# Optimization experiments

Measured on AMD Instinct MI355X. Metric: run time of the kernel, lower is better.

## Reference

```python
import jax, jax.numpy as jnp
import numpy as np

I, H = 16, 32  # input_size, hidden_size


def _rnn_layer(x, W_ih, W_hh, b_ih, b_hh):
    # x: [B, T, D] -> outputs [B, T, H] of tanh RNN layer
    B, T, _ = x.shape
    # precompute input projection for all timesteps: [B, T, H]
    xp = jnp.einsum('btd,hd->bth', x, W_ih) + b_ih + b_hh

    def step(h, xpt):
        h = jnp.tanh(xpt + h @ W_hh.T)
        return h, h

    h0 = jnp.zeros((B, H), dtype=x.dtype)
    _, ys = jax.lax.scan(step, h0, jnp.swapaxes(xp, 0, 1))  # ys: [T, B, H]
    return jnp.swapaxes(ys, 0, 1)


def setup_inputs() -> dict:
    key = jax.random.key(0)
    ks = jax.random.split(key, 11)
    B, T = 4096, 512
    s0 = 1.0 / np.sqrt(H)  # PyTorch RNN init bound
    u = lambda k, shape: jax.random.uniform(k, shape, jnp.float32, -s0, s0)
    return {
        'x': jax.random.normal(ks[0], (B, T, I), jnp.float32),
        'W_ih0': u(ks[1], (H, I)), 'W_hh0': u(ks[2], (H, H)),
        'b_ih0': u(ks[3], (H,)), 'b_hh0': u(ks[4], (H,)),
        'W_ih1': u(ks[5], (H, H)), 'W_hh1': u(ks[6], (H, H)),
        'b_ih1': u(ks[7], (H,)), 'b_hh1': u(ks[8], (H,)),
        'fc_w': u(ks[9], (1, H)), 'fc_b': u(ks[10], (1,)),
    }


def reference(x, W_ih0, W_hh0, b_ih0, b_hh0, W_ih1, W_hh1, b_ih1, b_hh1, fc_w, fc_b):
    h1 = _rnn_layer(x, W_ih0, W_hh0, b_ih0, b_hh0)   # [B, T, H]
    h2 = _rnn_layer(h1, W_ih1, W_hh1, b_ih1, b_hh1)  # [B, T, H]
    last = h2[:, -1, :]                               # [B, H]
    logits = last @ fc_w.T + fc_b                     # [B, 1]
    return logits
```

## Files before the change

kernel.cpp:

```cpp
#include <hip/hip_runtime.h>

#define T_DIM 512
#define I_DIM 16
#define B_DIM 4096
#define K_CH 32
#define COLS 8
#define SCL 2.885390081777927f

typedef _Float16 f16x8 __attribute__((ext_vector_type(8)));
typedef float f32x4 __attribute__((ext_vector_type(4)));
typedef __fp16 hf2v __attribute__((ext_vector_type(2)));

union Frag { f16x8 v; __fp16 e[8]; uint4 u; };

__device__ __forceinline__ float tanh_s(float u) {
    float e = __builtin_amdgcn_exp2f(u);
    return fmaf(-2.f, __builtin_amdgcn_rcpf(e + 1.f), 1.f);
}

__device__ __forceinline__ f16x8 pack8(float a0, float a1, float a2, float a3,
                                       float b0, float b1, float b2, float b3) {
    Frag f;
    hf2v p0 = __builtin_amdgcn_cvt_pkrtz(a0, a1);
    hf2v p1 = __builtin_amdgcn_cvt_pkrtz(a2, a3);
    hf2v p2 = __builtin_amdgcn_cvt_pkrtz(b0, b1);
    hf2v p3 = __builtin_amdgcn_cvt_pkrtz(b2, b3);
    f.e[0] = p0[0]; f.e[1] = p0[1]; f.e[2] = p1[0]; f.e[3] = p1[1];
    f.e[4] = p2[0]; f.e[5] = p2[1]; f.e[6] = p3[0]; f.e[7] = p3[1];
    return f.v;
}
__device__ __forceinline__ f16x8 tanhpack_s(f32x4 a, f32x4 b) {
    return pack8(tanh_s(a[0]), tanh_s(a[1]), tanh_s(a[2]), tanh_s(a[3]),
                 tanh_s(b[0]), tanh_s(b[1]), tanh_s(b[2]), tanh_s(b[3]));
}
__device__ __forceinline__ f16x8 loadWq32s(const float* W, int row, int g) {
    float4 a = *reinterpret_cast<const float4*>(W + row * 32 + 4 * g);
    float4 b = *reinterpret_cast<const float4*>(W + row * 32 + 16 + 4 * g);
    return pack8(a.x*SCL, a.y*SCL, a.z*SCL, a.w*SCL, b.x*SCL, b.y*SCL, b.z*SCL, b.w*SCL);
}
__device__ __forceinline__ f16x8 loadWq16s(const float* W, int row, int g) {
    float4 a = *reinterpret_cast<const float4*>(W + row * 16 + 4 * g);
    return pack8(a.x*SCL, a.y*SCL, a.z*SCL, a.w*SCL, 0.f, 0.f, 0.f, 0.f);
}

__global__ void __launch_bounds__(128)
rnn2_pc2_kernel(const float* __restrict__ x,
                const float* __restrict__ Wih0, const float* __restrict__ Whh0,
                const float* __restrict__ bih0, const float* __restrict__ bhh0,
                const float* __restrict__ Wih1, const float* __restrict__ Whh1,
                const float* __restrict__ bih1, const float* __restrict__ bhh1,
                const float* __restrict__ fcw, const float* __restrict__ fcb,
                float* __restrict__ out)
{
    const int tid = threadIdx.x;
    const int l   = tid & 63;
    const int wid = tid >> 6;
    const int c   = l & 15;
    const int g   = l >> 4;
    const int rowbase = blockIdx.x * COLS;

    __shared__ __fp16 ring[2][K_CH][64][8];

    f16x8 wT0[2], wT1[2];
    f32x4 bC[2];
    Frag  h1f;
    f32x4 Xacc[2];
    float4 xpA, xpB;
    const float* xlane = nullptr;
    float h20=0.f,h21=0.f,h22=0.f,h23=0.f,h24=0.f,h25=0.f,h26=0.f,h27=0.f;
    Frag h2f; h2f.u = make_uint4(0u, 0u, 0u, 0u);

    if (wid == 0) {
#pragma unroll
        for (int tt = 0; tt < 2; ++tt) {
            const int row = c + 16 * tt;
            wT0[tt] = loadWq32s(Whh0, row, g);
            wT1[tt] = loadWq16s(Wih0, row, g);
            const int r0 = 4 * g + 16 * tt;
            float4 bi = *reinterpret_cast<const float4*>(bih0 + r0);
            float4 bh = *reinterpret_cast<const float4*>(bhh0 + r0);
            bC[tt][0] = (bi.x + bh.x) * SCL; bC[tt][1] = (bi.y + bh.y) * SCL;
            bC[tt][2] = (bi.z + bh.z) * SCL; bC[tt][3] = (bi.w + bh.w) * SCL;
        }
        const size_t xcol = rowbase + (c & (COLS - 1));
        xlane = x + xcol * (size_t)(T_DIM * I_DIM) + 4 * g;
    } else {
#pragma unroll
        for (int tt = 0; tt < 2; ++tt) {
            const int row = c + 16 * tt;
            wT0[tt] = loadWq32s(Wih1, row, g);
            wT1[tt] = loadWq32s(Whh1, row, g);
            const int r0 = 4 * g + 16 * tt;
            float4 bi = *reinterpret_cast<const float4*>(bih1 + r0);
            float4 bh = *reinterpret_cast<const float4*>(bhh1 + r0);
            bC[tt][0] = (bi.x + bh.x) * SCL; bC[tt][1] = (bi.y + bh.y) * SCL;
            bC[tt][2] = (bi.z + bh.z) * SCL; bC[tt][3] = (bi.w + bh.w) * SCL;
        }
    }

#define PSTEP(t, P)                                                                         \
    {                                                                                       \
        f32x4 D0a = __builtin_amdgcn_mfma_f32_16x16x32_f16(wT0[0], h1f.v, Xacc[0], 0,0,0);  \
        f32x4 D0b = __builtin_amdgcn_mfma_f32_16x16x32_f16(wT0[1], h1f.v, Xacc[1], 0,0,0);  \
        Frag xf; xf.v = pack8((P).x, (P).y, (P).z, (P).w, 0.f, 0.f, 0.f, 0.f);              \
        const int tn = ((t) + 3 < T_DIM) ? (t) + 3 : (T_DIM - 1);                           \
        (P) = *reinterpret_cast<const float4*>(xlane + (size_t)tn * I_DIM);                 \
        h1f.v = tanhpack_s(D0a, D0b);                                                       \
        *reinterpret_cast<uint4*>(&ring[((t) / K_CH) & 1][(t) & (K_CH - 1)][l][0]) = h1f.u; \
        Xacc[0] = __builtin_amdgcn_mfma_f32_16x16x32_f16(wT1[0], xf.v, bC[0], 0,0,0);       \
        Xacc[1] = __builtin_amdgcn_mfma_f32_16x16x32_f16(wT1[1], xf.v, bC[1], 0,0,0);       \
    }

#pragma unroll 1
    for (int p = 0; p <= T_DIM / K_CH; ++p) {
        if (wid == 0 && p < T_DIM / K_CH) {
            if (p == 0) {
                float4 x0 = *reinterpret_cast<const float4*>(xlane + 0 * I_DIM);
                Frag xf0; xf0.v = pack8(x0.x, x0.y, x0.z, x0.w, 0.f, 0.f, 0.f, 0.f);
                f32x4 Da = __builtin_amdgcn_mfma_f32_16x16x32_f16(wT1[0], xf0.v, bC[0], 0,0,0);
                f32x4 Db = __builtin_amdgcn_mfma_f32_16x16x32_f16(wT1[1], xf0.v, bC[1], 0,0,0);
                h1f.v = tanhpack_s(Da, Db);
                *reinterpret_cast<uint4*>(&ring[0][0][l][0]) = h1f.u;
                float4 x1 = *reinterpret_cast<const float4*>(xlane + 1 * I_DIM);
                Frag xf1; xf1.v = pack8(x1.x, x1.y, x1.z, x1.w, 0.f, 0.f, 0.f, 0.f);
                Xacc[0] = __builtin_amdgcn_mfma_f32_16x16x32_f16(wT1[0], xf1.v, bC[0], 0,0,0);
                Xacc[1] = __builtin_amdgcn_mfma_f32_16x16x32_f16(wT1[1], xf1.v, bC[1], 0,0,0);
                f32x4 D0a = __builtin_amdgcn_mfma_f32_16x16x32_f16(wT0[0], h1f.v, Xacc[0], 0,0,0);
                f32x4 D0b = __builtin_amdgcn_mfma_f32_16x16x32_f16(wT0[1], h1f.v, Xacc[1], 0,0,0);
                float4 x2 = *reinterpret_cast<const float4*>(xlane + 2 * I_DIM);
                h1f.v = tanhpack_s(D0a, D0b);
                *reinterpret_cast<uint4*>(&ring[0][1][l][0]) = h1f.u;
                Frag xf2; xf2.v = pack8(x2.x, x2.y, x2.z, x2.w, 0.f, 0.f, 0.f, 0.f);
                Xacc[0] = __builtin_amdgcn_mfma_f32_16x16x32_f16(wT1[0], xf2.v, bC[0], 0,0,0);
                Xacc[1] = __builtin_amdgcn_mfma_f32_16x16x32_f16(wT1[1], xf2.v, bC[1], 0,0,0);
                xpA = *reinterpret_cast<const float4*>(xlane + 3 * I_DIM);
                xpB = *reinterpret_cast<const float4*>(xlane + 4 * I_DIM);
#pragma unroll 2
                for (int s = 2; s < K_CH; s += 2) { PSTEP(s, xpA) PSTEP(s + 1, xpB) }
            } else {
                const int t0 = p * K_CH;
#pragma unroll 2
                for (int s = 0; s < K_CH; s += 2) { PSTEP(t0 + s, xpA) PSTEP(t0 + s + 1, xpB) }
            }
        }
        if (wid == 1 && p >= 1) {
            const int cp  = p - 1;
            const int buf = cp & 1;
            Frag hB; hB.u = *reinterpret_cast<const uint4*>(&ring[buf][0][l][0]);
            f32x4 pd1a = __builtin_amdgcn_mfma_f32_16x16x32_f16(wT0[0], hB.v, bC[0], 0,0,0);
            f32x4 pd1b = __builtin_amdgcn_mfma_f32_16x16x32_f16(wT0[1], hB.v, bC[1], 0,0,0);
#pragma unroll 2
            for (int s = 0; s < K_CH; ++s) {
                f32x4 D1a = __builtin_amdgcn_mfma_f32_16x16x32_f16(wT1[0], h2f.v, pd1a, 0,0,0);
                f32x4 D1b = __builtin_amdgcn_mfma_f32_16x16x32_f16(wT1[1], h2f.v, pd1b, 0,0,0);
                const int sn = (s + 1 < K_CH) ? s + 1 : s;
                hB.u = *reinterpret_cast<const uint4*>(&ring[buf][sn][l][0]);
                pd1a = __builtin_amdgcn_mfma_f32_16x16x32_f16(wT0[0], hB.v, bC[0], 0,0,0);
                pd1b = __builtin_amdgcn_mfma_f32_16x16x32_f16(wT0[1], hB.v, bC[1], 0,0,0);
                h20 = tanh_s(D1a[0]); h21 = tanh_s(D1a[1]);
                h22 = tanh_s(D1a[2]); h23 = tanh_s(D1a[3]);
                h24 = tanh_s(D1b[0]); h25 = tanh_s(D1b[1]);
                h26 = tanh_s(D1b[2]); h27 = tanh_s(D1b[3]);
                h2f.v = pack8(h20, h21, h22, h23, h24, h25, h26, h27);
            }
        }
        __syncthreads();
    }
#undef PSTEP

    if (wid == 1) {
        float4 fw0 = *reinterpret_cast<const float4*>(fcw + 4 * g);
        float4 fw1 = *reinterpret_cast<const float4*>(fcw + 16 + 4 * g);
        float part = fw0.x * h20 + fw0.y * h21 + fw0.z * h22 + fw0.w * h23
                   + fw1.x * h24 + fw1.y * h25 + fw1.z * h26 + fw1.w * h27;
        part += __shfl_xor(part, 16, 64);
        part += __shfl_xor(part, 32, 64);
        if (l < COLS) out[rowbase + l] = part + fcb[0];
    }
}

extern "C" void kernel_launch(void* const* d_in, const int* in_sizes, int n_in,
                              void* d_out, int out_size, void* d_ws, size_t ws_size,
                              hipStream_t stream) {
    const float* x    = (const float*)d_in[0];
    const float* Wih0 = (const float*)d_in[1];
    const float* Whh0 = (const float*)d_in[2];
    const float* bih0 = (const float*)d_in[3];
    const float* bhh0 = (const float*)d_in[4];
    const float* Wih1 = (const float*)d_in[5];
    const float* Whh1 = (const float*)d_in[6];
    const float* bih1 = (const float*)d_in[7];
    const float* bhh1 = (const float*)d_in[8];
    const float* fcw  = (const float*)d_in[9];
    const float* fcb  = (const float*)d_in[10];
    float* out = (float*)d_out;

    dim3 grid(B_DIM / COLS);
    rnn2_pc2_kernel<<<grid, 128, 0, stream>>>(x, Wih0, Whh0, bih0, bhh0,
                                              Wih1, Whh1, bih1, bhh1,
                                              fcw, fcb, out);
}
```

Before: 98.02 us.

## Interleave two independent batch groups per wave to hide recurrent latency

Each block now handles 16 batch rows as two independent 8-row chains (A and B), and each wave interleaves the two recurrences so the MFMA and tanh latency of one chain overlaps with the other. The chunk size is halved to 16 so the doubled shared-memory ring stays the same size, and input prefetch depth is raised to four steps per chain. The grid is halved, which reduces the number of waves available to the scheduler and raises register pressure.

```diff
diff --git a/kernel.cpp b/kernel.cpp
--- a/kernel.cpp
+++ b/kernel.cpp
@@ -3,8 +3,9 @@
 #define T_DIM 512
 #define I_DIM 16
 #define B_DIM 4096
-#define K_CH 32
-#define COLS 8
+#define K_CH 16
+#define NCH  (T_DIM / K_CH)
+#define PF   4
 #define SCL 2.885390081777927f
 
 typedef _Float16 f16x8 __attribute__((ext_vector_type(8)));
@@ -17,7 +18,6 @@
     float e = __builtin_amdgcn_exp2f(u);
     return fmaf(-2.f, __builtin_amdgcn_rcpf(e + 1.f), 1.f);
 }
-
 __device__ __forceinline__ f16x8 pack8(float a0, float a1, float a2, float a3,
                                        float b0, float b1, float b2, float b3) {
     Frag f;
@@ -44,31 +44,33 @@
 }
 
 __global__ void __launch_bounds__(128)
-rnn2_pc2_kernel(const float* __restrict__ x,
-                const float* __restrict__ Wih0, const float* __restrict__ Whh0,
-                const float* __restrict__ bih0, const float* __restrict__ bhh0,
-                const float* __restrict__ Wih1, const float* __restrict__ Whh1,
-                const float* __restrict__ bih1, const float* __restrict__ bhh1,
-                const float* __restrict__ fcw, const float* __restrict__ fcb,
-                float* __restrict__ out)
+rnn2_dual_pc_kernel(const float* __restrict__ x,
+                    const float* __restrict__ Wih0, const float* __restrict__ Whh0,
+                    const float* __restrict__ bih0, const float* __restrict__ bhh0,
+                    const float* __restrict__ Wih1, const float* __restrict__ Whh1,
+                    const float* __restrict__ bih1, const float* __restrict__ bhh1,
+                    const float* __restrict__ fcw, const float* __restrict__ fcb,
+                    float* __restrict__ out)
 {
     const int tid = threadIdx.x;
     const int l   = tid & 63;
     const int wid = tid >> 6;
     const int c   = l & 15;
     const int g   = l >> 4;
-    const int rowbase = blockIdx.x * COLS;
-
-    __shared__ __fp16 ring[2][K_CH][64][8];
+    const int rowA = blockIdx.x * 16;
+    __shared__ __fp16 ring[2][2][K_CH][64][8];
 
     f16x8 wT0[2], wT1[2];
     f32x4 bC[2];
-    Frag  h1f;
-    f32x4 Xacc[2];
-    float4 xpA, xpB;
-    const float* xlane = nullptr;
-    float h20=0.f,h21=0.f,h22=0.f,h23=0.f,h24=0.f,h25=0.f,h26=0.f,h27=0.f;
-    Frag h2f; h2f.u = make_uint4(0u, 0u, 0u, 0u);
+    Frag h1A, h1B;
+    f32x4 XaccA[2], XaccB[2];
+    float4 xa0, xa1, xa2, xa3, xb0, xb1, xb2, xb3;
+    const float *xlA = nullptr, *xlB = nullptr;
+    float hA0=0.f,hA1=0.f,hA2=0.f,hA3=0.f,hA4=0.f,hA5=0.f,hA6=0.f,hA7=0.f;
+    float hB0=0.f,hB1=0.f,hB2=0.f,hB3=0.f,hB4=0.f,hB5=0.f,hB6=0.f,hB7=0.f;
+    Frag h2A, h2B;
+    h2A.u = make_uint4(0u,0u,0u,0u);
+    h2B.u = make_uint4(0u,0u,0u,0u);
 
     if (wid == 0) {
 #pragma unroll
@@ -82,8 +84,8 @@
             bC[tt][0] = (bi.x + bh.x) * SCL; bC[tt][1] = (bi.y + bh.y) * SCL;
             bC[tt][2] = (bi.z + bh.z) * SCL; bC[tt][3] = (bi.w + bh.w) * SCL;
         }
-        const size_t xcol = rowbase + (c & (COLS - 1));
-        xlane = x + xcol * (size_t)(T_DIM * I_DIM) + 4 * g;
+        xlA = x + (size_t)(rowA + (c & 7)) * (T_DIM * I_DIM) + 4 * g;
+        xlB = xlA + (size_t)8 * (T_DIM * I_DIM);
     } else {
 #pragma unroll
         for (int tt = 0; tt < 2; ++tt) {
@@ -98,70 +100,109 @@
         }
     }
 
-#define PSTEP(t, P)                                                                         \
-    {                                                                                       \
-        f32x4 D0a = __builtin_amdgcn_mfma_f32_16x16x32_f16(wT0[0], h1f.v, Xacc[0], 0,0,0);  \
-        f32x4 D0b = __builtin_amdgcn_mfma_f32_16x16x32_f16(wT0[1], h1f.v, Xacc[1], 0,0,0);  \
-        Frag xf; xf.v = pack8((P).x, (P).y, (P).z, (P).w, 0.f, 0.f, 0.f, 0.f);              \
-        const int tn = ((t) + 3 < T_DIM) ? (t) + 3 : (T_DIM - 1);                           \
-        (P) = *reinterpret_cast<const float4*>(xlane + (size_t)tn * I_DIM);                 \
-        h1f.v = tanhpack_s(D0a, D0b);                                                       \
-        *reinterpret_cast<uint4*>(&ring[((t) / K_CH) & 1][(t) & (K_CH - 1)][l][0]) = h1f.u; \
-        Xacc[0] = __builtin_amdgcn_mfma_f32_16x16x32_f16(wT1[0], xf.v, bC[0], 0,0,0);       \
-        Xacc[1] = __builtin_amdgcn_mfma_f32_16x16x32_f16(wT1[1], xf.v, bC[1], 0,0,0);       \
+#define PSTEP(t, P, H1, XA, XL, CH)                                                          \
+    {                                                                                        \
+        f32x4 D0a = __builtin_amdgcn_mfma_f32_16x16x32_f16(wT0[0], (H1).v, (XA)[0], 0,0,0);  \
+        f32x4 D0b = __builtin_amdgcn_mfma_f32_16x16x32_f16(wT0[1], (H1).v, (XA)[1], 0,0,0);  \
+        Frag xf; xf.v = pack8((P).x, (P).y, (P).z, (P).w, 0.f, 0.f, 0.f, 0.f);               \
+        const int tn = ((t) + PF + 1 < T_DIM) ? (t) + PF + 1 : (T_DIM - 1);                  \
+        (P) = *reinterpret_cast<const float4*>((XL) + (size_t)tn * I_DIM);                   \
+        (H1).v = tanhpack_s(D0a, D0b);                                                       \
+        *reinterpret_cast<uint4*>(&ring[CH][((t) / K_CH) & 1][(t) & (K_CH - 1)][l][0]) = (H1).u; \
+        (XA)[0] = __builtin_amdgcn_mfma_f32_16x16x32_f16(wT1[0], xf.v, bC[0], 0,0,0);        \
+        (XA)[1] = __builtin_amdgcn_mfma_f32_16x16x32_f16(wT1[1], xf.v, bC[1], 0,0,0);        \
     }
 
 #pragma unroll 1
-    for (int p = 0; p <= T_DIM / K_CH; ++p) {
-        if (wid == 0 && p < T_DIM / K_CH) {
+    for (int p = 0; p <= NCH; ++p) {
+        if (wid == 0 && p < NCH) {
             if (p == 0) {
-                float4 x0 = *reinterpret_cast<const float4*>(xlane + 0 * I_DIM);
-                Frag xf0; xf0.v = pack8(x0.x, x0.y, x0.z, x0.w, 0.f, 0.f, 0.f, 0.f);
-                f32x4 Da = __builtin_amdgcn_mfma_f32_16x16x32_f16(wT1[0], xf0.v, bC[0], 0,0,0);
-                f32x4 Db = __builtin_amdgcn_mfma_f32_16x16x32_f16(wT1[1], xf0.v, bC[1], 0,0,0);
-                h1f.v = tanhpack_s(Da, Db);
-                *reinterpret_cast<uint4*>(&ring[0][0][l][0]) = h1f.u;
-                float4 x1 = *reinterpret_cast<const float4*>(xlane + 1 * I_DIM);
-                Frag xf1; xf1.v = pack8(x1.x, x1.y, x1.z, x1.w, 0.f, 0.f, 0.f, 0.f);
-                Xacc[0] = __builtin_amdgcn_mfma_f32_16x16x32_f16(wT1[0], xf1.v, bC[0], 0,0,0);
-                Xacc[1] = __builtin_amdgcn_mfma_f32_16x16x32_f16(wT1[1], xf1.v, bC[1], 0,0,0);
-                f32x4 D0a = __builtin_amdgcn_mfma_f32_16x16x32_f16(wT0[0], h1f.v, Xacc[0], 0,0,0);
-                f32x4 D0b = __builtin_amdgcn_mfma_f32_16x16x32_f16(wT0[1], h1f.v, Xacc[1], 0,0,0);
-                float4 x2 = *reinterpret_cast<const float4*>(xlane + 2 * I_DIM);
-                h1f.v = tanhpack_s(D0a, D0b);
-                *reinterpret_cast<uint4*>(&ring[0][1][l][0]) = h1f.u;
-                Frag xf2; xf2.v = pack8(x2.x, x2.y, x2.z, x2.w, 0.f, 0.f, 0.f, 0.f);
-                Xacc[0] = __builtin_amdgcn_mfma_f32_16x16x32_f16(wT1[0], xf2.v, bC[0], 0,0,0);
-                Xacc[1] = __builtin_amdgcn_mfma_f32_16x16x32_f16(wT1[1], xf2.v, bC[1], 0,0,0);
-                xpA = *reinterpret_cast<const float4*>(xlane + 3 * I_DIM);
-                xpB = *reinterpret_cast<const float4*>(xlane + 4 * I_DIM);
-#pragma unroll 2
-                for (int s = 2; s < K_CH; s += 2) { PSTEP(s, xpA) PSTEP(s + 1, xpB) }
+#pragma unroll
+                for (int t = 0; t < PF; ++t) {
+                    float4 qa = *reinterpret_cast<const float4*>(xlA + (size_t)t * I_DIM);
+                    float4 qb = *reinterpret_cast<const float4*>(xlB + (size_t)t * I_DIM);
+                    Frag ga; ga.v = pack8(qa.x, qa.y, qa.z, qa.w, 0.f, 0.f, 0.f, 0.f);
+                    Frag gb; gb.v = pack8(qb.x, qb.y, qb.z, qb.w, 0.f, 0.f, 0.f, 0.f);
+                    f32x4 XA0 = __builtin_amdgcn_mfma_f32_16x16x32_f16(wT1[0], ga.v, bC[0], 0,0,0);
+                    f32x4 XA1 = __builtin_amdgcn_mfma_f32_16x16x32_f16(wT1[1], ga.v, bC[1], 0,0,0);
+                    f32x4 XB0 = __builtin_amdgcn_mfma_f32_16x16x32_f16(wT1[0], gb.v, bC[0], 0,0,0);
+                    f32x4 XB1 = __builtin_amdgcn_mfma_f32_16x16x32_f16(wT1[1], gb.v, bC[1], 0,0,0);
+                    f32x4 DA0, DA1, DB0, DB1;
+                    if (t == 0) { DA0 = XA0; DA1 = XA1; DB0 = XB0; DB1 = XB1; }
+                    else {
+                        DA0 = __builtin_amdgcn_mfma_f32_16x16x32_f16(wT0[0], h1A.v, XA0, 0,0,0);
+                        DA1 = __builtin_amdgcn_mfma_f32_16x16x32_f16(wT0[1], h1A.v, XA1, 0,0,0);
+                        DB0 = __builtin_amdgcn_mfma_f32_16x16x32_f16(wT0[0], h1B.v, XB0, 0,0,0);
+                        DB1 = __builtin_amdgcn_mfma_f32_16x16x32_f16(wT0[1], h1B.v, XB1, 0,0,0);
+                    }
+                    h1A.v = tanhpack_s(DA0, DA1);
+                    h1B.v = tanhpack_s(DB0, DB1);
+                    *reinterpret_cast<uint4*>(&ring[0][0][t][l][0]) = h1A.u;
+                    *reinterpret_cast<uint4*>(&ring[1][0][t][l][0]) = h1B.u;
+                }
+                {
+                    float4 qa = *reinterpret_cast<const float4*>(xlA + (size_t)PF * I_DIM);
+                    float4 qb = *reinterpret_cast<const float4*>(xlB + (size_t)PF * I_DIM);
+                    Frag ga; ga.v = pack8(qa.x, qa.y, qa.z, qa.w, 0.f, 0.f, 0.f, 0.f);
+                    Frag gb; gb.v = pack8(qb.x, qb.y, qb.z, qb.w, 0.f, 0.f, 0.f, 0.f);
+                    XaccA[0] = __builtin_amdgcn_mfma_f32_16x16x32_f16(wT1[0], ga.v, bC[0], 0,0,0);
+                    XaccA[1] = __builtin_amdgcn_mfma_f32_16x16x32_f16(wT1[1], ga.v, bC[1], 0,0,0);
+                    XaccB[0] = __builtin_amdgcn_mfma_f32_16x16x32_f16(wT1[0], gb.v, bC[0], 0,0,0);
+                    XaccB[1] = __builtin_amdgcn_mfma_f32_16x16x32_f16(wT1[1], gb.v, bC[1], 0,0,0);
+                }
+                xa0 = *reinterpret_cast<const float4*>(xlA + (PF + 1) * I_DIM);
+                xa1 = *reinterpret_cast<const float4*>(xlA + (PF + 2) * I_DIM);
+                xa2 = *reinterpret_cast<const float4*>(xlA + (PF + 3) * I_DIM);
+                xa3 = *reinterpret_cast<const float4*>(xlA + (PF + 4) * I_DIM);
+                xb0 = *reinterpret_cast<const float4*>(xlB + (PF + 1) * I_DIM);
+                xb1 = *reinterpret_cast<const float4*>(xlB + (PF + 2) * I_DIM);
+                xb2 = *reinterpret_cast<const float4*>(xlB + (PF + 3) * I_DIM);
+                xb3 = *reinterpret_cast<const float4*>(xlB + (PF + 4) * I_DIM);
+#pragma unroll 1
+                for (int sg = PF; sg < K_CH; sg += 4) {
+                    PSTEP(sg + 0, xa0, h1A, XaccA, xlA, 0) PSTEP(sg + 0, xb0, h1B, XaccB, xlB, 1)
+                    PSTEP(sg + 1, xa1, h1A, XaccA, xlA, 0) PSTEP(sg + 1, xb1, h1B, XaccB, xlB, 1)
+                    PSTEP(sg + 2, xa2, h1A, XaccA, xlA, 0) PSTEP(sg + 2, xb2, h1B, XaccB, xlB, 1)
+                    PSTEP(sg + 3, xa3, h1A, XaccA, xlA, 0) PSTEP(sg + 3, xb3, h1B, XaccB, xlB, 1)
+                }
             } else {
                 const int t0 = p * K_CH;
-#pragma unroll 2
-                for (int s = 0; s < K_CH; s += 2) { PSTEP(t0 + s, xpA) PSTEP(t0 + s + 1, xpB) }
+#pragma unroll 1
+                for (int sg = 0; sg < K_CH; sg += 4) {
+                    PSTEP(t0 + sg + 0, xa0, h1A, XaccA, xlA, 0) PSTEP(t0 + sg + 0, xb0, h1B, XaccB, xlB, 1)
+                    PSTEP(t0 + sg + 1, xa1, h1A, XaccA, xlA, 0) PSTEP(t0 + sg + 1, xb1, h1B, XaccB, xlB, 1)
+                    PSTEP(t0 + sg + 2, xa2, h1A, XaccA, xlA, 0) PSTEP(t0 + sg + 2, xb2, h1B, XaccB, xlB, 1)
+                    PSTEP(t0 + sg + 3, xa3, h1A, XaccA, xlA, 0) PSTEP(t0 + sg + 3, xb3, h1B, XaccB, xlB, 1)
+                }
             }
         }
         if (wid == 1 && p >= 1) {
-            const int cp  = p - 1;
-            const int buf = cp & 1;
-            Frag hB; hB.u = *reinterpret_cast<const uint4*>(&ring[buf][0][l][0]);
-            f32x4 pd1a = __builtin_amdgcn_mfma_f32_16x16x32_f16(wT0[0], hB.v, bC[0], 0,0,0);
-            f32x4 pd1b = __builtin_amdgcn_mfma_f32_16x16x32_f16(wT0[1], hB.v, bC[1], 0,0,0);
+            const int buf = (p - 1) & 1;
+            Frag rA; rA.u = *reinterpret_cast<const uint4*>(&ring[0][buf][0][l][0]);
+            f32x4 pdAa = __builtin_amdgcn_mfma_f32_16x16x32_f16(wT0[0], rA.v, bC[0], 0,0,0);
+            f32x4 pdAb = __builtin_amdgcn_mfma_f32_16x16x32_f16(wT0[1], rA.v, bC[1], 0,0,0);
+            Frag rB; rB.u = *reinterpret_cast<const uint4*>(&ring[1][buf][0][l][0]);
+            f32x4 pdBa = __builtin_amdgcn_mfma_f32_16x16x32_f16(wT0[0], rB.v, bC[0], 0,0,0);
+            f32x4 pdBb = __builtin_amdgcn_mfma_f32_16x16x32_f16(wT0[1], rB.v, bC[1], 0,0,0);
 #pragma unroll 2
             for (int s = 0; s < K_CH; ++s) {
-                f32x4 D1a = __builtin_amdgcn_mfma_f32_16x16x32_f16(wT1[0], h2f.v, pd1a, 0,0,0);
-                f32x4 D1b = __builtin_amdgcn_mfma_f32_16x16x32_f16(wT1[1], h2f.v, pd1b, 0,0,0);
+                f32x4 DAa = __builtin_amdgcn_mfma_f32_16x16x32_f16(wT1[0], h2A.v, pdAa, 0,0,0);
+                f32x4 DAb = __builtin_amdgcn_mfma_f32_16x16x32_f16(wT1[1], h2A.v, pdAb, 0,0,0);
+                f32x4 DBa = __builtin_amdgcn_mfma_f32_16x16x32_f16(wT1[0], h2B.v, pdBa, 0,0,0);
+                f32x4 DBb = __builtin_amdgcn_mfma_f32_16x16x32_f16(wT1[1], h2B.v, pdBb, 0,0,0);
                 const int sn = (s + 1 < K_CH) ? s + 1 : s;
-                hB.u = *reinterpret_cast<const uint4*>(&ring[buf][sn][l][0]);
-                pd1a = __builtin_amdgcn_mfma_f32_16x16x32_f16(wT0[0], hB.v, bC[0], 0,0,0);
-                pd1b = __builtin_amdgcn_mfma_f32_16x16x32_f16(wT0[1], hB.v, bC[1], 0,0,0);
-                h20 = tanh_s(D1a[0]); h21 = tanh_s(D1a[1]);
-                h22 = tanh_s(D1a[2]); h23 = tanh_s(D1a[3]);
-                h24 = tanh_s(D1b[0]); h25 = tanh_s(D1b[1]);
-                h26 = tanh_s(D1b[2]); h27 = tanh_s(D1b[3]);
-                h2f.v = pack8(h20, h21, h22, h23, h24, h25, h26, h27);
+                rA.u = *reinterpret_cast<const uint4*>(&ring[0][buf][sn][l][0]);
+                pdAa = __builtin_amdgcn_mfma_f32_16x16x32_f16(wT0[0], rA.v, bC[0], 0,0,0);
+                pdAb = __builtin_amdgcn_mfma_f32_16x16x32_f16(wT0[1], rA.v, bC[1], 0,0,0);
+                rB.u = *reinterpret_cast<const uint4*>(&ring[1][buf][sn][l][0]);
+                pdBa = __builtin_amdgcn_mfma_f32_16x16x32_f16(wT0[0], rB.v, bC[0], 0,0,0);
+                pdBb = __builtin_amdgcn_mfma_f32_16x16x32_f16(wT0[1], rB.v, bC[1], 0,0,0);
+                hA0 = tanh_s(DAa[0]); hA1 = tanh_s(DAa[1]); hA2 = tanh_s(DAa[2]); hA3 = tanh_s(DAa[3]);
+                hA4 = tanh_s(DAb[0]); hA5 = tanh_s(DAb[1]); hA6 = tanh_s(DAb[2]); hA7 = tanh_s(DAb[3]);
+                h2A.v = pack8(hA0, hA1, hA2, hA3, hA4, hA5, hA6, hA7);
+                hB0 = tanh_s(DBa[0]); hB1 = tanh_s(DBa[1]); hB2 = tanh_s(DBa[2]); hB3 = tanh_s(DBa[3]);
+                hB4 = tanh_s(DBb[0]); hB5 = tanh_s(DBb[1]); hB6 = tanh_s(DBb[2]); hB7 = tanh_s(DBb[3]);
+                h2B.v = pack8(hB0, hB1, hB2, hB3, hB4, hB5, hB6, hB7);
             }
         }
         __syncthreads();
@@ -171,11 +212,18 @@
     if (wid == 1) {
         float4 fw0 = *reinterpret_cast<const float4*>(fcw + 4 * g);
         float4 fw1 = *reinterpret_cast<const float4*>(fcw + 16 + 4 * g);
-        float part = fw0.x * h20 + fw0.y * h21 + fw0.z * h22 + fw0.w * h23
-                   + fw1.x * h24 + fw1.y * h25 + fw1.z * h26 + fw1.w * h27;
-        part += __shfl_xor(part, 16, 64);
-        part += __shfl_xor(part, 32, 64);
-        if (l < COLS) out[rowbase + l] = part + fcb[0];
+        float pA = fw0.x * hA0 + fw0.y * hA1 + fw0.z * hA2 + fw0.w * hA3
+                 + fw1.x * hA4 + fw1.y * hA5 + fw1.z * hA6 + fw1.w * hA7;
+        float pB = fw0.x * hB0 + fw0.y * hB1 + fw0.z * hB2 + fw0.w * hB3
+                 + fw1.x * hB4 + fw1.y * hB5 + fw1.z * hB6 + fw1.w * hB7;
+        pA += __shfl_xor(pA, 16, 64);
+        pA += __shfl_xor(pA, 32, 64);
+        pB += __shfl_xor(pB, 16, 64);
+        pB += __shfl_xor(pB, 32, 64);
+        if (l < 8) {
+            out[rowA + l]     = pA + fcb[0];
+            out[rowA + 8 + l] = pB + fcb[0];
+        }
     }
 }
 
@@ -195,8 +243,8 @@
     const float* fcb  = (const float*)d_in[10];
     float* out = (float*)d_out;
 
-    dim3 grid(B_DIM / COLS);
-    rnn2_pc2_kernel<<<grid, 128, 0, stream>>>(x, Wih0, Whh0, bih0, bhh0,
-                                              Wih1, Whh1, bih1, bhh1,
-                                              fcw, fcb, out);
-}
+    dim3 grid(B_DIM / 16);
+    rnn2_dual_pc_kernel<<<grid, 128, 0, stream>>>(x, Wih0, Whh0, bih0, bhh0,
+                                                  Wih1, Whh1, bih1, bhh1,
+                                                  fcw, fcb, out);
+}
```

After: 161.8 us. +65.1%, slower.
